# Performance work log

Hardware: AMD Instinct MI355X
Metric: run time of the kernel (lower is better)

Reference implementation:

```python
import jax, jax.numpy as jnp
import numpy as np

D_MODEL = 512
N_HEADS = 8
D_FF = 2048

def _linear_params(key, d_in, d_out):
    kw, kb = jax.random.split(key)
    bound = 1.0 / np.sqrt(d_in)
    W = jax.random.uniform(kw, (d_in, d_out), minval=-bound, maxval=bound, dtype=jnp.float32)
    b = jax.random.uniform(kb, (d_out,), minval=-bound, maxval=bound, dtype=jnp.float32)
    return W, b

def setup_inputs() -> dict:
    key = jax.random.key(0)
    ks = jax.random.split(key, 7)
    x = jax.random.normal(ks[0], (4, 2048, D_MODEL), dtype=jnp.float32)
    Wq, bq = _linear_params(ks[1], D_MODEL, D_MODEL)
    Wk, bk = _linear_params(ks[2], D_MODEL, D_MODEL)
    Wv, bv = _linear_params(ks[3], D_MODEL, D_MODEL)
    W1, b1 = _linear_params(ks[4], D_MODEL, D_FF)
    W2, b2 = _linear_params(ks[5], D_FF, D_MODEL)
    g1 = jnp.ones((D_MODEL,), jnp.float32); be1 = jnp.zeros((D_MODEL,), jnp.float32)
    g2 = jnp.ones((D_MODEL,), jnp.float32); be2 = jnp.zeros((D_MODEL,), jnp.float32)
    return {"x": x, "Wq": Wq, "bq": bq, "Wk": Wk, "bk": bk, "Wv": Wv, "bv": bv,
            "W1": W1, "b1": b1, "W2": W2, "b2": b2,
            "g1": g1, "be1": be1, "g2": g2, "be2": be2}

def _layernorm(x, g, b, eps=1e-5):
    mu = jnp.mean(x, axis=-1, keepdims=True)
    var = jnp.mean(jnp.square(x - mu), axis=-1, keepdims=True)
    return (x - mu) * jax.lax.rsqrt(var + eps) * g + b

def reference(x, Wq, bq, Wk, bk, Wv, bv, W1, b1, W2, b2, g1, be1, g2, be2):
    B, S, D = x.shape
    H = N_HEADS
    Dh = D // H
    residual = x
    xn = _layernorm(x, g1, be1)
    # [B,S,D] -> [B,H,S,Dh]
    q = (xn @ Wq + bq).reshape(B, S, H, Dh).transpose(0, 2, 1, 3)
    k = (xn @ Wk + bk).reshape(B, S, H, Dh).transpose(0, 2, 1, 3)
    v = (xn @ Wv + bv).reshape(B, S, H, Dh).transpose(0, 2, 1, 3)
    # sigmoid pointwise attention, scaled by sqrt(d_model) (not head dim)
    scores = jnp.einsum('bhsd,bhtd->bhst', q, k) / jnp.sqrt(jnp.float32(D))
    attn = jax.nn.sigmoid(scores)
    out = jnp.einsum('bhst,bhtd->bhsd', attn, v)
    out = out.transpose(0, 2, 1, 3).reshape(B, S, D)
    x = residual + out  # dropout=0 (eval)
    residual = x
    xn = _layernorm(x, g2, be2)
    ffn = jax.nn.relu(xn @ W1 + b1) @ W2 + b2
    return residual + ffn
```

## Files before the change

### kernel.cpp

```cpp
#include <hip/hip_runtime.h>
#include <hip/hip_bf16.h>
#include <math.h>

#define D_MODEL 512
#define N_HEADS 8
#define D_HEAD 64
#define D_FF 2048
#define SEQ 2048
#define BATCH 4
#define NTOK (BATCH * SEQ)
#define QSCALE 0.04419417382415922f
#define QSCALE_L2E (-QSCALE * 1.44269504089f)

typedef unsigned short ushort_t;
typedef __attribute__((ext_vector_type(8))) short short8;
typedef __attribute__((ext_vector_type(4))) float float4v;

static __device__ __forceinline__ ushort_t f2bf(float f) {
    union { float f; unsigned int i; } c; c.f = f;
    unsigned int i = c.i;
    unsigned int r = (i + 0x7FFFu + ((i >> 16) & 1u)) >> 16;
    return (ushort_t)r;
}

static __device__ __forceinline__ unsigned int pack2bf(float a, float b) {
    union { __hip_bfloat162 h; unsigned int u; } c;
    c.h = __float22bfloat162_rn(make_float2(a, b));
    return c.u;
}

static __device__ __forceinline__ float sig2(float x) {
    return __builtin_amdgcn_rcpf(1.0f + __builtin_amdgcn_exp2f(x));
}

__global__ __launch_bounds__(256) void k_prep_weights(const float* __restrict__ Wq,
                                                      const float* __restrict__ Wk,
                                                      const float* __restrict__ Wv,
                                                      const float* __restrict__ W1,
                                                      const float* __restrict__ W2,
                                                      ushort_t* __restrict__ Wqkvt,
                                                      ushort_t* __restrict__ W1t,
                                                      ushort_t* __restrict__ W2t) {
    __shared__ ushort_t tile[64][66];
    int bid = blockIdx.x;
    const float* src; ushort_t* dst; int K, N, tk, tn;
    if (bid < 192) {
        int m = bid >> 6, r = bid & 63;
        src = (m == 0) ? Wq : ((m == 1) ? Wk : Wv);
        dst = Wqkvt + (size_t)m * 512 * 512; K = 512; N = 512; tk = r >> 3; tn = r & 7;
    } else if (bid < 448) {
        int r = bid - 192; src = W1; dst = W1t; K = 512; N = 2048; tk = r >> 5; tn = r & 31;
    } else {
        int r = bid - 448; src = W2; dst = W2t; K = 2048; N = 512; tk = r >> 3; tn = r & 7;
    }
    int k0 = tk * 64, n0 = tn * 64;
    int rr = threadIdx.x >> 6, c = threadIdx.x & 63;
#pragma unroll
    for (int i = 0; i < 16; i++) {
        int row = i * 4 + rr;
        tile[row][c] = f2bf(src[(size_t)(k0 + row) * N + n0 + c]);
    }
    __syncthreads();
#pragma unroll
    for (int i = 0; i < 16; i++) {
        int row = i * 4 + rr;
        dst[(size_t)(n0 + row) * K + k0 + c] = tile[c][row];
    }
}

__global__ __launch_bounds__(256) void k_layernorm(const float* __restrict__ X,
                                                   const float* __restrict__ g,
                                                   const float* __restrict__ be,
                                                   ushort_t* __restrict__ Out) {
    int row  = blockIdx.x * 4 + (threadIdx.x >> 6);
    int lane = threadIdx.x & 63;
    const float* x = X + (size_t)row * D_MODEL + lane * 8;
    float4 v0 = ((const float4*)x)[0];
    float4 v1 = ((const float4*)x)[1];
    float vals[8] = {v0.x, v0.y, v0.z, v0.w, v1.x, v1.y, v1.z, v1.w};
    float s = 0.f, sq = 0.f;
#pragma unroll
    for (int j = 0; j < 8; j++) { s += vals[j]; sq += vals[j] * vals[j]; }
#pragma unroll
    for (int off = 32; off; off >>= 1) { s += __shfl_xor(s, off); sq += __shfl_xor(sq, off); }
    float mu  = s * (1.0f / D_MODEL);
    float var = sq * (1.0f / D_MODEL) - mu * mu;
    float inv = rsqrtf(var + 1e-5f);
    const float* gp  = g  + lane * 8;
    const float* bp  = be + lane * 8;
    float4 g0 = ((const float4*)gp)[0], g1v = ((const float4*)gp)[1];
    float4 b0 = ((const float4*)bp)[0], b1v = ((const float4*)bp)[1];
    float gs[8] = {g0.x, g0.y, g0.z, g0.w, g1v.x, g1v.y, g1v.z, g1v.w};
    float bs[8] = {b0.x, b0.y, b0.z, b0.w, b1v.x, b1v.y, b1v.z, b1v.w};
    ushort_t o[8];
#pragma unroll
    for (int j = 0; j < 8; j++) o[j] = f2bf((vals[j] - mu) * inv * gs[j] + bs[j]);
    ushort_t* op = Out + (size_t)row * D_MODEL + lane * 8;
    *(uint4*)op = *(uint4*)o;
}

static __device__ __forceinline__ void stage_tile(const ushort_t* __restrict__ G, int K,
                                                  ushort_t* L, int nchunks, int koff,
                                                  int w, int l) {
#pragma unroll
    for (int n = w; n < nchunks; n += 4) {
        const ushort_t* g = G + (size_t)(n * 16 + (l >> 2)) * K + koff + (l & 3) * 8;
        __builtin_amdgcn_global_load_lds((const __attribute__((address_space(1))) void*)g,
                                         (__attribute__((address_space(3))) void*)(L + n * 512),
                                         16, 0, 0);
    }
}

template <int JW>
static __device__ __forceinline__ void gemm_core2(const ushort_t* __restrict__ A,
                                                  const ushort_t* __restrict__ Bt,
                                                  int K, int m0, int n0,
                                                  ushort_t* As, ushort_t* Bs,
                                                  float4v acc[4][JW]) {
    const int BBUF = JW * 1024;
    int t = threadIdx.x, w = t >> 6, l = t & 63, q = l >> 4, lm = l & 15;
    int mb = (w & 1) * 64, nb = (w >> 1) * (JW * 16);
    const ushort_t* Ab = A + (size_t)m0 * K;
    const ushort_t* Bb = Bt + (size_t)n0 * K;
    int T = K >> 5;

    stage_tile(Ab, K, As, 8, 0, w, l);
    stage_tile(Bb, K, Bs, 2 * JW, 0, w, l);
    __syncthreads();

    for (int kt = 0; kt < T; kt++) {
        int cur = kt & 1;
        if (kt + 1 < T) {
            stage_tile(Ab, K, As + (1 - cur) * 4096, 8, (kt + 1) * 32, w, l);
            stage_tile(Bb, K, Bs + (1 - cur) * BBUF, 2 * JW, (kt + 1) * 32, w, l);
        }
        const ushort_t* asb = As + cur * 4096;
        const ushort_t* bsb = Bs + cur * BBUF;
        short8 a[4], b[JW];
#pragma unroll
        for (int i = 0; i < 4; i++) a[i] = *(const short8*)&asb[(mb + 16 * i + lm) * 32 + q * 8];
#pragma unroll
        for (int j = 0; j < JW; j++) b[j] = *(const short8*)&bsb[(nb + 16 * j + lm) * 32 + q * 8];
#pragma unroll
        for (int i = 0; i < 4; i++)
#pragma unroll
            for (int j = 0; j < JW; j++)
                acc[i][j] = __builtin_amdgcn_mfma_f32_16x16x32_bf16(a[i], b[j], acc[i][j], 0, 0, 0);
        __syncthreads();
    }
}

__global__ __launch_bounds__(256) void k_gemm_qkv(const ushort_t* __restrict__ A,
                                                  const ushort_t* __restrict__ Bt,
                                                  const float* __restrict__ bq,
                                                  const float* __restrict__ bk,
                                                  const float* __restrict__ bv,
                                                  ushort_t* __restrict__ qb,
                                                  ushort_t* __restrict__ kb,
                                                  ushort_t* __restrict__ vt) {
    __shared__ __align__(16) ushort_t As[8192];
    __shared__ __align__(16) ushort_t Bs[8192];
    int m0 = blockIdx.x * 128, n0 = blockIdx.y * 128;
    float4v acc[4][4];
#pragma unroll
    for (int i = 0; i < 4; i++)
#pragma unroll
        for (int j = 0; j < 4; j++) acc[i][j] = (float4v){0.f, 0.f, 0.f, 0.f};
    gemm_core2<4>(A, Bt, D_MODEL, m0, n0, As, Bs, acc);

    int t = threadIdx.x, w = t >> 6, l = t & 63, q = l >> 4, lm = l & 15;
    int mb = (w & 1) * 64, nb = (w >> 1) * 64;
    int mat = n0 >> 9, c0 = n0 & 511;
    const float* bias = (mat == 0) ? bq : ((mat == 1) ? bk : bv);
#pragma unroll
    for (int j = 0; j < 4; j++) {
        int cl = c0 + nb + 16 * j + lm;
        int hh = cl >> 6, dh = cl & 63;
        float bvv = bias[cl];
#pragma unroll
        for (int i = 0; i < 4; i++) {
            int mr0 = m0 + mb + 16 * i + q * 4;
            int bb = mr0 >> 11, ss0 = mr0 & (SEQ - 1);
            if (mat == 2) {
                union { ushort_t s[4]; uint2 v; } pk;
#pragma unroll
                for (int r = 0; r < 4; r++) pk.s[r] = f2bf(acc[i][j][r] + bvv);
                *(uint2*)&vt[((size_t)(bb * N_HEADS + hh) * D_HEAD + dh) * SEQ + ss0] = pk.v;
            } else {
                ushort_t* dst = (mat == 0) ? qb : kb;
                float sc = (mat == 0) ? QSCALE_L2E : 1.0f;
#pragma unroll
                for (int r = 0; r < 4; r++)
                    dst[((size_t)(bb * N_HEADS + hh) * SEQ + ss0 + r) * D_HEAD + dh] =
                        f2bf((acc[i][j][r] + bvv) * sc);
            }
        }
    }
}

__global__ __launch_bounds__(256) void k_gemm_ffn1(const ushort_t* __restrict__ A,
                                                   const ushort_t* __restrict__ Bt,
                                                   const float* __restrict__ b1,
                                                   ushort_t* __restrict__ hb) {
    __shared__ __align__(16) ushort_t As[8192];
    __shared__ __align__(16) ushort_t Bs[8192];
    int m0 = blockIdx.x * 128, n0 = blockIdx.y * 128;
    float4v acc[4][4];
#pragma unroll
    for (int i = 0; i < 4; i++)
#pragma unroll
        for (int j = 0; j < 4; j++) acc[i][j] = (float4v){0.f, 0.f, 0.f, 0.f};
    gemm_core2<4>(A, Bt, D_MODEL, m0, n0, As, Bs, acc);

    int t = threadIdx.x, w = t >> 6, l = t & 63, q = l >> 4, lm = l & 15;
    int mb = (w & 1) * 64, nb = (w >> 1) * 64;
#pragma unroll
    for (int j = 0; j < 4; j++) {
        int cl = n0 + nb + 16 * j + lm;
        float bvv = b1[cl];
#pragma unroll
        for (int i = 0; i < 4; i++) {
            int mr0 = m0 + mb + 16 * i + q * 4;
#pragma unroll
            for (int r = 0; r < 4; r++)
                hb[(size_t)(mr0 + r) * D_FF + cl] = f2bf(fmaxf(acc[i][j][r] + bvv, 0.f));
        }
    }
}

__global__ __launch_bounds__(256) void k_gemm_ffn2(const ushort_t* __restrict__ A,
                                                   const ushort_t* __restrict__ Bt,
                                                   const float* __restrict__ b2,
                                                   const float* __restrict__ res,
                                                   float* __restrict__ out) {
    __shared__ __align__(16) ushort_t As[8192];
    __shared__ __align__(16) ushort_t Bs[4096];
    int m0 = blockIdx.x * 128, n0 = blockIdx.y * 64;
    float4v acc[4][2];
#pragma unroll
    for (int i = 0; i < 4; i++)
#pragma unroll
        for (int j = 0; j < 2; j++) acc[i][j] = (float4v){0.f, 0.f, 0.f, 0.f};
    gemm_core2<2>(A, Bt, D_FF, m0, n0, As, Bs, acc);

    int t = threadIdx.x, w = t >> 6, l = t & 63, q = l >> 4, lm = l & 15;
    int mb = (w & 1) * 64, nb = (w >> 1) * 32;
#pragma unroll
    for (int j = 0; j < 2; j++) {
        int cl = n0 + nb + 16 * j + lm;
        float bvv = b2[cl];
#pragma unroll
        for (int i = 0; i < 4; i++) {
            int mr0 = m0 + mb + 16 * i + q * 4;
#pragma unroll
            for (int r = 0; r < 4; r++) {
                size_t idx = (size_t)(mr0 + r) * D_MODEL + cl;
                out[idx] = acc[i][j][r] + bvv + res[idx];
            }
        }
    }
}

__global__ __launch_bounds__(512) void k_attention(const ushort_t* __restrict__ Q,
                                                   const ushort_t* __restrict__ Kb,
                                                   const ushort_t* __restrict__ Vt,
                                                   const float* __restrict__ X,
                                                   float* __restrict__ Y) {
    __shared__ __align__(16) char smem[57344];
    ushort_t* Ks = (ushort_t*)smem;
    ushort_t* Vs = (ushort_t*)(smem + 18432);
    ushort_t* Ps = (ushort_t*)(smem + 36864);
    float*  Osum = (float*)smem;

    int bh = blockIdx.y;
    int b = bh >> 3, h = bh & 7;
    size_t base = (size_t)bh * SEQ * D_HEAD;
    int s0 = blockIdx.x * 128;
    int t = threadIdx.x, w = t >> 6, l = t & 63, q = l >> 4, lm = l & 15;
    int g = w >> 1, th = w & 1;
    int srow = t >> 3, sc = (t & 7) * 8;
    ushort_t* Pw = Ps + w * 1280;

    short8 qf[2][2];
#pragma unroll
    for (int nt = 0; nt < 2; nt++)
#pragma unroll
        for (int kc = 0; kc < 2; kc++) {
            const ushort_t* qg = Q + base + (size_t)(s0 + 32 * g + 16 * nt + lm) * D_HEAD + kc * 32 + q * 8;
            uint4 u = *(const uint4*)qg;
            qf[nt][kc] = *(const short8*)&u;
        }

    float4v o[2][4];
#pragma unroll
    for (int nt = 0; nt < 2; nt++)
#pragma unroll
        for (int dj = 0; dj < 4; dj++) o[nt][dj] = (float4v){0.f, 0.f, 0.f, 0.f};

    uint4 kr, vr;
    const ushort_t* kg0 = Kb + base + (size_t)srow * D_HEAD + sc;
    const ushort_t* vg0 = Vt + base + (size_t)srow * SEQ + sc;

    kr = *(const uint4*)(kg0); vr = *(const uint4*)(vg0);
    *(uint4*)&Ks[srow * 72 + sc] = kr; *(uint4*)&Vs[srow * 72 + sc] = vr;
    kr = *(const uint4*)(kg0 + 64 * D_HEAD); vr = *(const uint4*)(vg0 + 64);
    __syncthreads();

    for (int tt = 0; tt < SEQ / 64; tt++) {
        int cur = tt & 1;
        const ushort_t* ksb = Ks + cur * 4608;
        const ushort_t* vsb = Vs + cur * 4608;
        short8 kf[2][2];
#pragma unroll
        for (int mt = 0; mt < 2; mt++)
#pragma unroll
            for (int kc = 0; kc < 2; kc++)
                kf[mt][kc] = *(const short8*)&ksb[(32 * th + 16 * mt + lm) * 72 + kc * 32 + q * 8];
        short8 vf[4];
#pragma unroll
        for (int dj = 0; dj < 4; dj++)
            vf[dj] = *(const short8*)&vsb[(16 * dj + lm) * 72 + th * 32 + q * 8];
        float4v st[2][2];
#pragma unroll
        for (int mt = 0; mt < 2; mt++)
#pragma unroll
            for (int nt = 0; nt < 2; nt++) st[mt][nt] = (float4v){0.f, 0.f, 0.f, 0.f};
#pragma unroll
        for (int kc = 0; kc < 2; kc++)
#pragma unroll
            for (int mt = 0; mt < 2; mt++)
#pragma unroll
                for (int nt = 0; nt < 2; nt++)
                    st[mt][nt] = __builtin_amdgcn_mfma_f32_16x16x32_bf16(kf[mt][kc], qf[nt][kc], st[mt][nt], 0, 0, 0);
#pragma unroll
        for (int mt = 0; mt < 2; mt++)
#pragma unroll
            for (int nt = 0; nt < 2; nt++) {
                uint2 pk;
                pk.x = pack2bf(sig2(st[mt][nt][0]), sig2(st[mt][nt][1]));
                pk.y = pack2bf(sig2(st[mt][nt][2]), sig2(st[mt][nt][3]));
                *(uint2*)&Pw[(16 * nt + lm) * 40 + 16 * mt + 4 * q] = pk;
            }
#pragma unroll
        for (int nt = 0; nt < 2; nt++) {
            short8 ap = *(const short8*)&Pw[(16 * nt + lm) * 40 + q * 8];
#pragma unroll
            for (int dj = 0; dj < 4; dj++)
                o[nt][dj] = __builtin_amdgcn_mfma_f32_16x16x32_bf16(ap, vf[dj], o[nt][dj], 0, 0, 0);
        }
        if (tt + 1 < SEQ / 64) {
            int nxt = 1 - cur;
            *(uint4*)&Ks[nxt * 4608 + srow * 72 + sc] = kr;
            *(uint4*)&Vs[nxt * 4608 + srow * 72 + sc] = vr;
            if (tt + 2 < SEQ / 64) {
                kr = *(const uint4*)(kg0 + (size_t)(tt + 2) * 64 * D_HEAD);
                vr = *(const uint4*)(vg0 + (tt + 2) * 64);
            }
        }
        __syncthreads();
    }

    __syncthreads();
    if (th == 0) {
#pragma unroll
        for (int nt = 0; nt < 2; nt++)
#pragma unroll
            for (int dj = 0; dj < 4; dj++)
#pragma unroll
                for (int r = 0; r < 4; r++)
                    Osum[(32 * g + 16 * nt + 4 * q + r) * 66 + 16 * dj + lm] = o[nt][dj][r];
    }
    __syncthreads();
    if (th == 1) {
#pragma unroll
        for (int nt = 0; nt < 2; nt++)
#pragma unroll
            for (int dj = 0; dj < 4; dj++)
#pragma unroll
                for (int r = 0; r < 4; r++)
                    Osum[(32 * g + 16 * nt + 4 * q + r) * 66 + 16 * dj + lm] += o[nt][dj][r];
    }
    __syncthreads();

    {
        int row = t >> 2, c0 = (t & 3) * 16;
        size_t gro = ((size_t)(b * SEQ + s0 + row)) * D_MODEL + h * D_HEAD + c0;
        const float* xp = X + gro;
        float* yp = Y + gro;
        const float* os = &Osum[row * 66 + c0];
#pragma unroll
        for (int i = 0; i < 4; i++) {
            float4 xv = *(const float4*)(xp + i * 4);
            float4 ov = *(const float4*)(os + i * 4);
            float4 rr;
            rr.x = xv.x + ov.x; rr.y = xv.y + ov.y;
            rr.z = xv.z + ov.z; rr.w = xv.w + ov.w;
            *(float4*)(yp + i * 4) = rr;
        }
    }
}

extern "C" void kernel_launch(void* const* d_in, const int* in_sizes, int n_in,
                              void* d_out, int out_size, void* d_ws, size_t ws_size,
                              hipStream_t stream) {
    const float* x   = (const float*)d_in[0];
    const float* Wq  = (const float*)d_in[1];
    const float* bq  = (const float*)d_in[2];
    const float* Wk  = (const float*)d_in[3];
    const float* bk  = (const float*)d_in[4];
    const float* Wv  = (const float*)d_in[5];
    const float* bv  = (const float*)d_in[6];
    const float* W1  = (const float*)d_in[7];
    const float* b1  = (const float*)d_in[8];
    const float* W2  = (const float*)d_in[9];
    const float* b2  = (const float*)d_in[10];
    const float* g1  = (const float*)d_in[11];
    const float* be1 = (const float*)d_in[12];
    const float* g2  = (const float*)d_in[13];
    const float* be2 = (const float*)d_in[14];
    float* out = (float*)d_out;

    char* p = (char*)d_ws;
    ushort_t* xn    = (ushort_t*)p; p += (size_t)NTOK * D_MODEL * 2;
    ushort_t* yn    = (ushort_t*)p; p += (size_t)NTOK * D_MODEL * 2;
    float*    y     = (float*)p;    p += (size_t)NTOK * D_MODEL * 4;
    ushort_t* qb    = (ushort_t*)p; p += (size_t)NTOK * D_MODEL * 2;
    ushort_t* kb    = (ushort_t*)p; p += (size_t)NTOK * D_MODEL * 2;
    ushort_t* vt    = (ushort_t*)p; p += (size_t)NTOK * D_MODEL * 2;
    ushort_t* hb    = (ushort_t*)p; p += (size_t)NTOK * D_FF * 2;
    ushort_t* Wqkvt = (ushort_t*)p; p += (size_t)3 * D_MODEL * D_MODEL * 2;
    ushort_t* W1t   = (ushort_t*)p; p += (size_t)D_MODEL * D_FF * 2;
    ushort_t* W2t   = (ushort_t*)p; p += (size_t)D_FF * D_MODEL * 2;

    k_prep_weights<<<704, 256, 0, stream>>>(Wq, Wk, Wv, W1, W2, Wqkvt, W1t, W2t);

    k_layernorm<<<NTOK / 4, 256, 0, stream>>>(x, g1, be1, xn);

    dim3 gq(NTOK / 128, (3 * D_MODEL) / 128);
    k_gemm_qkv<<<gq, 256, 0, stream>>>(xn, Wqkvt, bq, bk, bv, qb, kb, vt);

    dim3 ga(SEQ / 128, BATCH * N_HEADS);
    k_attention<<<ga, 512, 0, stream>>>(qb, kb, vt, x, y);

    k_layernorm<<<NTOK / 4, 256, 0, stream>>>(y, g2, be2, yn);

    dim3 g1d(NTOK / 128, D_FF / 128);
    k_gemm_ffn1<<<g1d, 256, 0, stream>>>(yn, W1t, b1, hb);
    dim3 g2d(NTOK / 128, D_MODEL / 64);
    k_gemm_ffn2<<<g2d, 256, 0, stream>>>(hb, W2t, b2, y, out);
}
```

Before: 245.1 us.

## Keep sigmoid probabilities in registers and feed PV MFMA directly, dropping LDS staging

```diff
diff --git a/kernel.cpp b/kernel.cpp
--- a/kernel.cpp
+++ b/kernel.cpp
@@ -14,6 +14,7 @@
 
 typedef unsigned short ushort_t;
 typedef __attribute__((ext_vector_type(8))) short short8;
+typedef __attribute__((ext_vector_type(4))) short short4v;
 typedef __attribute__((ext_vector_type(4))) float float4v;
 
 static __device__ __forceinline__ ushort_t f2bf(float f) {
@@ -266,10 +267,9 @@
                                                    const ushort_t* __restrict__ Vt,
                                                    const float* __restrict__ X,
                                                    float* __restrict__ Y) {
-    __shared__ __align__(16) char smem[57344];
+    __shared__ __align__(16) char smem[36864];
     ushort_t* Ks = (ushort_t*)smem;
     ushort_t* Vs = (ushort_t*)(smem + 18432);
-    ushort_t* Ps = (ushort_t*)(smem + 36864);
     float*  Osum = (float*)smem;
 
     int bh = blockIdx.y;
@@ -279,7 +279,6 @@
     int t = threadIdx.x, w = t >> 6, l = t & 63, q = l >> 4, lm = l & 15;
     int g = w >> 1, th = w & 1;
     int srow = t >> 3, sc = (t & 7) * 8;
-    ushort_t* Pw = Ps + w * 1280;
 
     short8 qf[2][2];
 #pragma unroll
@@ -316,10 +315,6 @@
 #pragma unroll
             for (int kc = 0; kc < 2; kc++)
                 kf[mt][kc] = *(const short8*)&ksb[(32 * th + 16 * mt + lm) * 72 + kc * 32 + q * 8];
-        short8 vf[4];
-#pragma unroll
-        for (int dj = 0; dj < 4; dj++)
-            vf[dj] = *(const short8*)&vsb[(16 * dj + lm) * 72 + th * 32 + q * 8];
         float4v st[2][2];
 #pragma unroll
         for (int mt = 0; mt < 2; mt++)
@@ -332,21 +327,27 @@
 #pragma unroll
                 for (int nt = 0; nt < 2; nt++)
                     st[mt][nt] = __builtin_amdgcn_mfma_f32_16x16x32_bf16(kf[mt][kc], qf[nt][kc], st[mt][nt], 0, 0, 0);
+        short4v pf[2][2];
 #pragma unroll
         for (int mt = 0; mt < 2; mt++)
 #pragma unroll
             for (int nt = 0; nt < 2; nt++) {
-                uint2 pk;
-                pk.x = pack2bf(sig2(st[mt][nt][0]), sig2(st[mt][nt][1]));
-                pk.y = pack2bf(sig2(st[mt][nt][2]), sig2(st[mt][nt][3]));
-                *(uint2*)&Pw[(16 * nt + lm) * 40 + 16 * mt + 4 * q] = pk;
-            }
-#pragma unroll
-        for (int nt = 0; nt < 2; nt++) {
-            short8 ap = *(const short8*)&Pw[(16 * nt + lm) * 40 + q * 8];
+                union { unsigned int u[2]; short4v v; } pk;
+                pk.u[0] = pack2bf(sig2(st[mt][nt][0]), sig2(st[mt][nt][1]));
+                pk.u[1] = pack2bf(sig2(st[mt][nt][2]), sig2(st[mt][nt][3]));
+                pf[mt][nt] = pk.v;
+            }
+#pragma unroll
+        for (int mt = 0; mt < 2; mt++) {
+            short4v vf[4];
 #pragma unroll
             for (int dj = 0; dj < 4; dj++)
-                o[nt][dj] = __builtin_amdgcn_mfma_f32_16x16x32_bf16(ap, vf[dj], o[nt][dj], 0, 0, 0);
+                vf[dj] = *(const short4v*)&vsb[(16 * dj + lm) * 72 + 32 * th + 16 * mt + 4 * q];
+#pragma unroll
+            for (int dj = 0; dj < 4; dj++)
+#pragma unroll
+                for (int nt = 0; nt < 2; nt++)
+                    o[nt][dj] = __builtin_amdgcn_mfma_f32_16x16x16bf16_1k(vf[dj], pf[mt][nt], o[nt][dj], 0, 0, 0);
         }
         if (tt + 1 < SEQ / 64) {
             int nxt = 1 - cur;
@@ -365,20 +366,23 @@
 #pragma unroll
         for (int nt = 0; nt < 2; nt++)
 #pragma unroll
-            for (int dj = 0; dj < 4; dj++)
-#pragma unroll
-                for (int r = 0; r < 4; r++)
-                    Osum[(32 * g + 16 * nt + 4 * q + r) * 66 + 16 * dj + lm] = o[nt][dj][r];
+            for (int dj = 0; dj < 4; dj++) {
+                float4v v = o[nt][dj];
+                *(float4*)&Osum[(32 * g + 16 * nt + lm) * 68 + 16 * dj + 4 * q] =
+                    make_float4(v[0], v[1], v[2], v[3]);
+            }
     }
     __syncthreads();
     if (th == 1) {
 #pragma unroll
         for (int nt = 0; nt < 2; nt++)
 #pragma unroll
-            for (int dj = 0; dj < 4; dj++)
-#pragma unroll
-                for (int r = 0; r < 4; r++)
-                    Osum[(32 * g + 16 * nt + 4 * q + r) * 66 + 16 * dj + lm] += o[nt][dj][r];
+            for (int dj = 0; dj < 4; dj++) {
+                float* p = &Osum[(32 * g + 16 * nt + lm) * 68 + 16 * dj + 4 * q];
+                float4 old = *(float4*)p;
+                float4v v = o[nt][dj];
+                *(float4*)p = make_float4(old.x + v[0], old.y + v[1], old.z + v[2], old.w + v[3]);
+            }
     }
     __syncthreads();
 
@@ -387,7 +391,7 @@
         size_t gro = ((size_t)(b * SEQ + s0 + row)) * D_MODEL + h * D_HEAD + c0;
         const float* xp = X + gro;
         float* yp = Y + gro;
-        const float* os = &Osum[row * 66 + c0];
+        const float* os = &Osum[row * 68 + c0];
 #pragma unroll
         for (int i = 0; i < 4; i++) {
             float4 xv = *(const float4*)(xp + i * 4);
```

Result: no change. 245.0 us (-0.0%).
